# Kernel tuning notes

Hardware: AMD Instinct MI355X
Metric: run time of the kernel (lower is better)

The kernel has to match this reference:

```python
import jax, jax.numpy as jnp
import numpy as np

B, T, H, S, OBS, ACT = 64, 256, 1024, 128, 1024, 32


def setup_inputs() -> dict:
    key = jax.random.key(0)
    ks = jax.random.split(key, 9)
    w = lambda k, shape, fan_in: jax.random.normal(k, shape, jnp.float32) / np.sqrt(fan_in).astype(np.float32)
    return {
        "obs": jax.random.normal(ks[0], (B, T, OBS), jnp.float32),
        "action": jax.random.normal(ks[1], (B, T, ACT), jnp.float32),
        "resets": jnp.zeros((B,), jnp.bool_),
        "noise": jax.random.normal(ks[2], (B, T, S), jnp.float32),
        # GRUCell params (PyTorch layout: gates ordered r,z,n)
        "w_ih": w(ks[3], (3 * H, S + ACT), S + ACT),
        "w_hh": w(ks[4], (3 * H, H), H),
        "b_ih": jnp.zeros((3 * H,), jnp.float32),
        "b_hh": jnp.zeros((3 * H,), jnp.float32),
        # prior MLP: H -> H//2 -> 2S
        "pr_w1": w(ks[5], (H // 2, H), H),
        "pr_b1": jnp.zeros((H // 2,), jnp.float32),
        "pr_w2": w(ks[6], (2 * S, H // 2), H // 2),
        "pr_b2": jnp.zeros((2 * S,), jnp.float32),
        # posterior MLP: (H+OBS) -> (H+OBS)//2 -> 2S
        "po_w1": w(ks[7], ((H + OBS) // 2, H + OBS), H + OBS),
        "po_b1": jnp.zeros(((H + OBS) // 2,), jnp.float32),
        "po_w2": w(ks[8], (2 * S, (H + OBS) // 2), (H + OBS) // 2),
        "po_b2": jnp.zeros((2 * S,), jnp.float32),
    }


def reference(obs, action, resets, noise, w_ih, w_hh, b_ih, b_hh,
              pr_w1, pr_b1, pr_w2, pr_b2, po_w1, po_b1, po_w2, po_b2):
    Bv, Tv, _ = obs.shape
    keep = (~resets).astype(obs.dtype)[:, None]  # [B,1]; multiplies h,z for t>0
    # prev_action: zeros at t=0, action[:, t-1] afterwards
    prev_act = jnp.concatenate([jnp.zeros_like(action[:, :1]), action[:, :-1]], axis=1)

    def step(carry, xs):
        h, z = carry
        a_t, o_t, n_t, t_pos = xs
        m = jnp.where(t_pos > 0, keep, jnp.ones_like(keep))
        h = h * m
        z = z * m
        x = jnp.concatenate([z, a_t], axis=-1)
        gi = x @ w_ih.T + b_ih
        gh = h @ w_hh.T + b_hh
        ir, iz, inn = jnp.split(gi, 3, axis=-1)
        hr, hz, hn = jnp.split(gh, 3, axis=-1)
        r = jax.nn.sigmoid(ir + hr)
        u = jax.nn.sigmoid(iz + hz)
        n = jnp.tanh(inn + r * hn)
        h = (1.0 - u) * n + u * h
        pp = jax.nn.relu(h @ pr_w1.T + pr_b1) @ pr_w2.T + pr_b2
        pm, ps = jnp.split(pp, 2, axis=-1)
        ps = jax.nn.softplus(ps) + 1e-6
        qp = jax.nn.relu(jnp.concatenate([h, o_t], axis=-1) @ po_w1.T + po_b1) @ po_w2.T + po_b2
        qm, qs = jnp.split(qp, 2, axis=-1)
        qs = jax.nn.softplus(qs) + 1e-6
        z = qm + qs * n_t  # reparameterized rsample
        return (h, z), (h, z, pm, ps, qm, qs)

    h0 = jnp.zeros((Bv, w_hh.shape[-1]), obs.dtype)
    z0 = jnp.zeros((Bv, noise.shape[-1]), obs.dtype)
    xs = (jnp.swapaxes(prev_act, 0, 1), jnp.swapaxes(obs, 0, 1),
          jnp.swapaxes(noise, 0, 1), jnp.arange(Tv))
    _, (hs, zs, pm, ps, qm, qs) = jax.lax.scan(step, (h0, z0), xs)
    h_seq = jnp.swapaxes(hs, 0, 1)  # [B,T,H]
    z_seq = jnp.swapaxes(zs, 0, 1)  # [B,T,S]
    to_last = lambda a: jnp.moveaxis(a, 0, -1)  # torch stacks dists along dim=-1 -> [B,S,T]
    return (to_last(pm), to_last(ps), to_last(qm), to_last(qs), h_seq, z_seq)
```

## Files before the change

### kernel.cpp

```cpp
#include <hip/hip_runtime.h>

#define B_ 64
#define T_ 256
#define H_ 1024
#define S_ 128
#define OBS_ 1024
#define ACT_ 32

typedef __attribute__((ext_vector_type(8))) short bf16x8;
typedef __attribute__((ext_vector_type(4))) float f32x4;

#define MFMA(a, b, c) __builtin_amdgcn_mfma_f32_16x16x32_bf16((a), (b), (c), 0, 0, 0)

__device__ __forceinline__ float bf2f(short s) {
    unsigned int u = ((unsigned int)(unsigned short)s) << 16;
    float f; __builtin_memcpy(&f, &u, 4); return f;
}
__device__ __forceinline__ short f2bf(float f) {
    unsigned int u; __builtin_memcpy(&u, &f, 4);
    unsigned int r = (u + 0x7fffu + ((u >> 16) & 1u)) >> 16;
    return (short)r;
}
__device__ __forceinline__ bf16x8 ld8(const short* p) { return *(const bf16x8*)p; }
__device__ __forceinline__ bf16x8 cvt8(const float* p) {
    bf16x8 r;
#pragma unroll
    for (int i = 0; i < 8; ++i) r[i] = f2bf(p[i]);
    return r;
}
__device__ __forceinline__ void sta8(short* p, unsigned long long v) {
    __hip_atomic_store((unsigned long long*)p, v, __ATOMIC_RELAXED, __HIP_MEMORY_SCOPE_AGENT);
}
__device__ __forceinline__ unsigned long long pk4(float4 v) {
    return (unsigned long long)(unsigned short)f2bf(v.x)
         | ((unsigned long long)(unsigned short)f2bf(v.y) << 16)
         | ((unsigned long long)(unsigned short)f2bf(v.z) << 32)
         | ((unsigned long long)(unsigned short)f2bf(v.w) << 48);
}
__device__ __forceinline__ float sigm(float x) { return 1.f / (1.f + __expf(-x)); }
__device__ __forceinline__ float tanh_f(float x) { return 1.f - 2.f / (__expf(2.f * x) + 1.f); }
__device__ __forceinline__ float splus(float x) { return (x > 20.f) ? x : log1pf(__expf(x)); }

__device__ __forceinline__ void gridbar(int* flags, int e) {
    __syncthreads();
    if (threadIdx.x == 0)
        __hip_atomic_store(&flags[blockIdx.x * 16], e, __ATOMIC_RELAXED, __HIP_MEMORY_SCOPE_AGENT);
    if (threadIdx.x < 64) {
        while (__hip_atomic_load(&flags[threadIdx.x * 16], __ATOMIC_RELAXED,
                                 __HIP_MEMORY_SCOPE_AGENT) < e)
            __builtin_amdgcn_s_sleep(1);
    }
    __builtin_amdgcn_fence(__ATOMIC_ACQUIRE, "agent");
    __syncthreads();
}

__global__ void f2bf_arr(const float* __restrict__ src, short* __restrict__ dst, int n4) {
    int i = blockIdx.x * blockDim.x + threadIdx.x;
    if (i < n4) {
        float4 v = ((const float4*)src)[i];
        short4 o;
        o.x = f2bf(v.x); o.y = f2bf(v.y); o.z = f2bf(v.z); o.w = f2bf(v.w);
        ((short4*)dst)[i] = o;
    }
}

__global__ __launch_bounds__(256) void obs_gemm(
    const float* __restrict__ obs, const short* __restrict__ po_w1,
    const float* __restrict__ po_b1, short* __restrict__ part) {
    const int t = blockIdx.x;
    const int rg = threadIdx.x >> 6, lane = threadIdx.x & 63;
    const int c = lane & 15, q = lane >> 4;
    bf16x8 afr[32];
    const float* ap = obs + ((size_t)(rg * 16 + c) * T_ + t) * OBS_;
#pragma unroll
    for (int kb = 0; kb < 32; ++kb) afr[kb] = cvt8(ap + kb * 32 + q * 8);
    for (int jt = 0; jt < 64; ++jt) {
        f32x4 acc = {0.f, 0.f, 0.f, 0.f};
        const short* wgt = po_w1 + (size_t)(jt * 16 + c) * 2048 + 1024;
#pragma unroll 8
        for (int kb = 0; kb < 32; ++kb) acc = MFMA(afr[kb], ld8(wgt + kb * 32 + q * 8), acc);
        const float bias = po_b1[jt * 16 + c];
#pragma unroll
        for (int e = 0; e < 4; ++e) {
            const int br = rg * 16 + q * 4 + e;
            part[((size_t)t * 64 + br) * 1024 + jt * 16 + c] = f2bf(acc[e] + bias);
        }
    }
}

__global__ __launch_bounds__(256, 1) void rssm_scan(
    const short* __restrict__ act_bf, const unsigned char* __restrict__ resets,
    const short* __restrict__ w_ih, const short* __restrict__ w_hh,
    const float* __restrict__ b_ih, const float* __restrict__ b_hh,
    const short* __restrict__ po_w1, const short* __restrict__ po_w2,
    const float* __restrict__ po_b2, const short* __restrict__ part,
    const float* __restrict__ noise,
    int* flags, short* h_bf, short* z_bf, short* poh,
    float* __restrict__ out_h, float* __restrict__ out_qm,
    float* __restrict__ out_qs, float* __restrict__ out_z) {
    extern __shared__ __align__(16) char smem[];
    bf16x8* wlds = (bf16x8*)smem;
    __shared__ __align__(16) float stg[64][20];
    const int tid = threadIdx.x, bid = blockIdx.x;
    const int rg = tid >> 6, lane = tid & 63, c = lane & 15, q = lane >> 4;
    const int j0 = bid * 16, m0 = rg * 16, arow = m0 + c, n = j0 + c;
    const int srow = tid >> 2, sseg = tid & 3;
    const bf16x8 zv8 = {0, 0, 0, 0, 0, 0, 0, 0};

    for (int i = 0; i < 32; ++i) {
        const int fid = i * 256 + tid;
        const int g = fid >> 11, kb = (fid >> 6) & 31, ln = fid & 63;
        const int cc = ln & 15, qq = ln >> 4;
        const short* src = (g == 0)
            ? po_w1 + (size_t)(j0 + cc) * 2048 + kb * 32 + qq * 8
            : w_hh + (size_t)((g - 1) * 1024 + j0 + cc) * 1024 + kb * 32 + qq * 8;
        wlds[fid] = ld8(src);
    }
    bf16x8* wih = wlds + 8192;
    for (int f = tid; f < 960; f += 256) {
        const int g = f / 320, rem = f % 320, kk = rem >> 6, ln = rem & 63;
        const int cc = ln & 15, qq = ln >> 4;
        wih[f] = ld8(w_ih + (size_t)(g * 1024 + j0 + cc) * 160 + kk * 32 + qq * 8);
    }
    __syncthreads();

    const bool rsA = resets[arow] != 0;
    bool rsR[4];
#pragma unroll
    for (int e = 0; e < 4; ++e) rsR[e] = resets[m0 + q * 4 + e] != 0;
    const float biR = b_ih[n], bhR = b_hh[n];
    const float biU = b_ih[1024 + n], bhU = b_hh[1024 + n];
    const float biN = b_ih[2048 + n], bhN = b_hh[2048 + n];
    const short* ha = h_bf + arow * 1024;
    const bf16x8* wPl = wlds;
    const bf16x8* wRl = wlds + 2048;
    const bf16x8* wUl = wlds + 4096;
    const bf16x8* wNl = wlds + 6144;
    const bf16x8* wiRl = wih;
    const bf16x8* wiUl = wih + 320;
    const bf16x8* wiNl = wih + 640;
    const int s2 = (bid < 8) ? j0 + c : 0;
    const short* wm = po_w2 + (size_t)s2 * 1024;
    const short* ws2 = po_w2 + (size_t)(128 + s2) * 1024;
    const float bM = (bid < 8) ? po_b2[s2] : 0.f;
    const float bS = (bid < 8) ? po_b2[128 + s2] : 0.f;

    f32x4 hp = {0.f, 0.f, 0.f, 0.f};
    f32x4 gR = {0.f, 0.f, 0.f, 0.f};
    f32x4 gU = {0.f, 0.f, 0.f, 0.f};
    f32x4 gN = {0.f, 0.f, 0.f, 0.f};
    f32x4 pinit;
#pragma unroll
    for (int e = 0; e < 4; ++e)
        pinit[e] = bf2f(part[((size_t)0 * 64 + m0 + q * 4 + e) * 1024 + n]);

    int ep = 1;
    for (int t = 0; t < T_; ++t) {
        f32x4 iR = {0.f, 0.f, 0.f, 0.f};
        f32x4 iU = iR, iN = iR;
        if (t > 0) {
            const short* za = z_bf + arow * 128;
            bf16x8 zfr[4];
#pragma unroll
            for (int kb = 0; kb < 4; ++kb) zfr[kb] = ld8(za + kb * 32 + q * 8);
            bf16x8 a2 = ld8(act_bf + (size_t)arow * (T_ * ACT_) + (size_t)(t - 1) * ACT_ + q * 8);
#pragma unroll
            for (int kb = 0; kb < 4; ++kb) {
                bf16x8 a = rsA ? zv8 : zfr[kb];
                iR = MFMA(a, wiRl[kb * 64 + lane], iR);
                iU = MFMA(a, wiUl[kb * 64 + lane], iU);
                iN = MFMA(a, wiNl[kb * 64 + lane], iN);
            }
            iR = MFMA(a2, wiRl[256 + lane], iR);
            iU = MFMA(a2, wiUl[256 + lane], iU);
            iN = MFMA(a2, wiNl[256 + lane], iN);
        }
#pragma unroll
        for (int e = 0; e < 4; ++e) {
            const float hpv = (t > 0 && rsR[e]) ? 0.f : hp[e];
            const float r = sigm(iR[e] + gR[e] + biR + bhR);
            const float u = sigm(iU[e] + gU[e] + biU + bhU);
            const float nn = tanh_f(iN[e] + biN + r * (gN[e] + bhN));
            const float hv = (1.f - u) * nn + u * hpv;
            hp[e] = hv;
            stg[m0 + q * 4 + e][c] = hv;
        }
        __syncthreads();
        {
            float4 hv4 = *(const float4*)&stg[srow][sseg * 4];
            sta8(h_bf + srow * 1024 + j0 + sseg * 4, pk4(hv4));
            *(float4*)(out_h + (size_t)srow * (T_ * H_) + (size_t)t * H_ + j0 + sseg * 4) = hv4;
        }
        gridbar(flags, ep++);
        float nz[4];
        {
            bf16x8 hfr[32];
#pragma unroll
            for (int kb = 0; kb < 32; ++kb) hfr[kb] = ld8(ha + kb * 32 + q * 8);
            f32x4 accP = pinit;
            if (t + 1 < T_) {
#pragma unroll
                for (int e = 0; e < 4; ++e)
                    pinit[e] = bf2f(part[((size_t)(t + 1) * 64 + m0 + q * 4 + e) * 1024 + n]);
            }
            if (bid < 8) {
#pragma unroll
                for (int e = 0; e < 4; ++e)
                    nz[e] = noise[(size_t)(m0 + q * 4 + e) * (T_ * S_) + (size_t)t * S_ + s2];
            }
            f32x4 nR = {0.f, 0.f, 0.f, 0.f};
            f32x4 nU = nR, nN = nR;
#pragma unroll 8
            for (int kb = 0; kb < 32; ++kb) {
                bf16x8 a = hfr[kb];
                bf16x8 am = rsA ? zv8 : a;
                accP = MFMA(a, wPl[kb * 64 + lane], accP);
                nR = MFMA(am, wRl[kb * 64 + lane], nR);
                nU = MFMA(am, wUl[kb * 64 + lane], nU);
                nN = MFMA(am, wNl[kb * 64 + lane], nN);
            }
            gR = nR; gU = nU; gN = nN;
#pragma unroll
            for (int e = 0; e < 4; ++e) stg[m0 + q * 4 + e][c] = fmaxf(accP[e], 0.f);
        }
        __syncthreads();
        {
            float4 v4 = *(const float4*)&stg[srow][sseg * 4];
            sta8(poh + srow * 1024 + j0 + sseg * 4, pk4(v4));
        }
        gridbar(flags, ep++);
        if (bid < 8) {
            bf16x8 pfr[32];
            const short* pa = poh + arow * 1024;
#pragma unroll
            for (int kb = 0; kb < 32; ++kb) pfr[kb] = ld8(pa + kb * 32 + q * 8);
            f32x4 aM = {0.f, 0.f, 0.f, 0.f};
            f32x4 aS = aM;
#pragma unroll 8
            for (int kb = 0; kb < 32; ++kb) {
                aM = MFMA(pfr[kb], ld8(wm + kb * 32 + q * 8), aM);
                aS = MFMA(pfr[kb], ld8(ws2 + kb * 32 + q * 8), aS);
            }
#pragma unroll
            for (int e = 0; e < 4; ++e) {
                const int row = m0 + q * 4 + e;
                const float qm = aM[e] + bM;
                const float qs = splus(aS[e] + bS) + 1e-6f;
                stg[row][c] = qm + qs * nz[e];
                out_qm[(size_t)row * (S_ * T_) + (size_t)s2 * T_ + t] = qm;
                out_qs[(size_t)row * (S_ * T_) + (size_t)s2 * T_ + t] = qs;
            }
            __syncthreads();
            {
                float4 z4 = *(const float4*)&stg[srow][sseg * 4];
                *(float4*)(out_z + (size_t)srow * (T_ * S_) + (size_t)t * S_ + j0 + sseg * 4) = z4;
                sta8(z_bf + srow * 128 + j0 + sseg * 4, pk4(z4));
            }
        }
        gridbar(flags, ep++);
    }
}

__global__ __launch_bounds__(256) void prior_mlp(
    const float* __restrict__ hseq, const short* __restrict__ pr_w1,
    const float* __restrict__ pr_b1, const short* __restrict__ pr_w2,
    const float* __restrict__ pr_b2, float* __restrict__ out_pm,
    float* __restrict__ out_ps) {
    __shared__ __align__(16) short hid[64][512];
    const int w = threadIdx.x >> 6;
    const int lane = threadIdx.x & 63;
    const int c = lane & 15, q = lane >> 4;
    const long rb0 = (long)blockIdx.x * 64;
    bf16x8 afr[32];
    const float* ap = hseq + (rb0 + w * 16 + c) * 1024;
#pragma unroll
    for (int kb = 0; kb < 32; ++kb) afr[kb] = cvt8(ap + kb * 32 + q * 8);
    for (int jt = 0; jt < 32; ++jt) {
        f32x4 acc = {0.f, 0.f, 0.f, 0.f};
        const short* wgt = pr_w1 + (size_t)(jt * 16 + c) * 1024;
#pragma unroll 8
        for (int kb = 0; kb < 32; ++kb) acc = MFMA(afr[kb], ld8(wgt + kb * 32 + q * 8), acc);
        const float bias = pr_b1[jt * 16 + c];
#pragma unroll
        for (int e = 0; e < 4; ++e)
            hid[w * 16 + q * 4 + e][jt * 16 + c] = f2bf(fmaxf(acc[e] + bias, 0.f));
    }
    __syncthreads();
    bf16x8 afr2[16];
#pragma unroll
    for (int kb = 0; kb < 16; ++kb) afr2[kb] = *(const bf16x8*)(&hid[w * 16 + c][kb * 32 + q * 8]);
    for (int jt = 0; jt < 16; ++jt) {
        f32x4 acc = {0.f, 0.f, 0.f, 0.f};
        const short* wgt = pr_w2 + (size_t)(jt * 16 + c) * 512;
#pragma unroll 8
        for (int kb = 0; kb < 16; ++kb) acc = MFMA(afr2[kb], ld8(wgt + kb * 32 + q * 8), acc);
        const int col = jt * 16 + c;
#pragma unroll
        for (int e = 0; e < 4; ++e) {
            const long rgidx = rb0 + w * 16 + q * 4 + e;
            const int b_ = (int)(rgidx >> 8), t_ = (int)(rgidx & 255);
            if (col < S_) {
                out_pm[(size_t)b_ * (S_ * T_) + (size_t)col * T_ + t_] = acc[e] + pr_b2[col];
            } else {
                out_ps[(size_t)b_ * (S_ * T_) + (size_t)(col - S_) * T_ + t_] =
                    splus(acc[e] + pr_b2[col]) + 1e-6f;
            }
        }
    }
}

extern "C" void kernel_launch(void* const* d_in, const int* in_sizes, int n_in,
                              void* d_out, int out_size, void* d_ws, size_t ws_size,
                              hipStream_t stream) {
    const float* obs = (const float*)d_in[0];
    const float* action = (const float*)d_in[1];
    const unsigned char* resets = (const unsigned char*)d_in[2];
    const float* noise = (const float*)d_in[3];
    const float* w_ih = (const float*)d_in[4];
    const float* w_hh = (const float*)d_in[5];
    const float* b_ih = (const float*)d_in[6];
    const float* b_hh = (const float*)d_in[7];
    const float* pr_w1 = (const float*)d_in[8];
    const float* pr_b1 = (const float*)d_in[9];
    const float* pr_w2 = (const float*)d_in[10];
    const float* pr_b2 = (const float*)d_in[11];
    const float* po_w1 = (const float*)d_in[12];
    const float* po_b1 = (const float*)d_in[13];
    const float* po_w2 = (const float*)d_in[14];
    const float* po_b2 = (const float*)d_in[15];

    float* out = (float*)d_out;
    const size_t BST = (size_t)B_ * S_ * T_;
    float* out_pm = out;
    float* out_ps = out + BST;
    float* out_qm = out + 2 * BST;
    float* out_qs = out + 3 * BST;
    float* out_h = out + 4 * BST;
    float* out_z = out + 4 * BST + (size_t)B_ * T_ * H_;

    char* w = (char*)d_ws;
    int* flags = (int*)w;
    short* h_bf = (short*)(w + 4096);
    short* z_bf = (short*)(w + 266240);
    short* poh = (short*)(w + 282624);
    short* act_bf = (short*)(w + 413696);
    short* w_ih_bf = (short*)(w + 1462272);
    short* w_hh_bf = (short*)(w + 2445312);
    short* po_w1_bf = (short*)(w + 8736768);
    short* po_w2_bf = (short*)(w + 12931072);
    short* pr_w1_bf = (short*)(w + 13455360);
    short* pr_w2_bf = (short*)(w + 14503936);
    short* part = (short*)(w + 14766080);

    static bool attr_set = false;
    if (!attr_set) {
        hipFuncSetAttribute(reinterpret_cast<const void*>(&rssm_scan),
                            hipFuncAttributeMaxDynamicSharedMemorySize, 146432);
        attr_set = true;
    }

    auto cvt = [&](const float* s, short* d, int n) {
        int n4 = n / 4;
        f2bf_arr<<<dim3((n4 + 255) / 256), 256, 0, stream>>>(s, d, n4);
    };
    cvt(action, act_bf, B_ * T_ * ACT_);
    cvt(w_ih, w_ih_bf, 3 * H_ * (S_ + ACT_));
    cvt(w_hh, w_hh_bf, 3 * H_ * H_);
    cvt(po_w1, po_w1_bf, 1024 * 2048);
    cvt(po_w2, po_w2_bf, 256 * 1024);
    cvt(pr_w1, pr_w1_bf, 512 * 1024);
    cvt(pr_w2, pr_w2_bf, 256 * 512);

    obs_gemm<<<dim3(256), 256, 0, stream>>>(obs, po_w1_bf, po_b1, part);

    rssm_scan<<<dim3(64), 256, 146432, stream>>>(
        act_bf, resets, w_ih_bf, w_hh_bf, b_ih, b_hh,
        po_w1_bf, po_w2_bf, po_b2, part, noise,
        flags, h_bf, z_bf, poh, out_h, out_qm, out_qs, out_z);

    prior_mlp<<<dim3(256), 256, 0, stream>>>(out_h, pr_w1_bf, pr_b1, pr_w2_bf, pr_b2,
                                             out_pm, out_ps);
}
```

Before: 11.93 ms.

## Drop grid-barrier acquire fence and stage posterior outputs for a separate transpose

Removes the agent-scope acquire fence from the software grid barrier. In its place, the cross-block buffers (h, z, posterior hidden) are read with relaxed agent-scope atomic loads, which avoids a cache invalidation at every one of the many per-step barriers. The strided per-timestep qm/qs stores inside the serial scan become contiguous writes into a staging buffer. That buffer reuses the already-consumed slice of the precomputed obs-projection buffer. A new transpose kernel then writes them to the [B,S,T] layout, which adds a launch and extra traffic but moves the scattered stores off the critical path. Correctness now depends on every cross-block read going through the atomic path and on the buffer aliasing order.

```diff
diff --git a/kernel.cpp b/kernel.cpp
--- a/kernel.cpp
+++ b/kernel.cpp
@@ -27,6 +27,13 @@
 #pragma unroll
     for (int i = 0; i < 8; ++i) r[i] = f2bf(p[i]);
     return r;
+}
+__device__ __forceinline__ bf16x8 lda8(const short* p) {
+    const unsigned long long* q8 = (const unsigned long long*)p;
+    union { unsigned long long q[2]; bf16x8 v; } u;
+    u.q[0] = __hip_atomic_load(q8, __ATOMIC_RELAXED, __HIP_MEMORY_SCOPE_AGENT);
+    u.q[1] = __hip_atomic_load(q8 + 1, __ATOMIC_RELAXED, __HIP_MEMORY_SCOPE_AGENT);
+    return u.v;
 }
 __device__ __forceinline__ void sta8(short* p, unsigned long long v) {
     __hip_atomic_store((unsigned long long*)p, v, __ATOMIC_RELAXED, __HIP_MEMORY_SCOPE_AGENT);
@@ -50,7 +57,6 @@
                                  __HIP_MEMORY_SCOPE_AGENT) < e)
             __builtin_amdgcn_s_sleep(1);
     }
-    __builtin_amdgcn_fence(__ATOMIC_ACQUIRE, "agent");
     __syncthreads();
 }
 
@@ -93,11 +99,10 @@
     const short* __restrict__ w_ih, const short* __restrict__ w_hh,
     const float* __restrict__ b_ih, const float* __restrict__ b_hh,
     const short* __restrict__ po_w1, const short* __restrict__ po_w2,
-    const float* __restrict__ po_b2, const short* __restrict__ part,
+    const float* __restrict__ po_b2, const short* part, float* qbuf,
     const float* __restrict__ noise,
     int* flags, short* h_bf, short* z_bf, short* poh,
-    float* __restrict__ out_h, float* __restrict__ out_qm,
-    float* __restrict__ out_qs, float* __restrict__ out_z) {
+    float* __restrict__ out_h, float* __restrict__ out_z) {
     extern __shared__ __align__(16) char smem[];
     bf16x8* wlds = (bf16x8*)smem;
     __shared__ __align__(16) float stg[64][20];
@@ -162,7 +167,7 @@
             const short* za = z_bf + arow * 128;
             bf16x8 zfr[4];
 #pragma unroll
-            for (int kb = 0; kb < 4; ++kb) zfr[kb] = ld8(za + kb * 32 + q * 8);
+            for (int kb = 0; kb < 4; ++kb) zfr[kb] = lda8(za + kb * 32 + q * 8);
             bf16x8 a2 = ld8(act_bf + (size_t)arow * (T_ * ACT_) + (size_t)(t - 1) * ACT_ + q * 8);
 #pragma unroll
             for (int kb = 0; kb < 4; ++kb) {
@@ -196,7 +201,7 @@
         {
             bf16x8 hfr[32];
 #pragma unroll
-            for (int kb = 0; kb < 32; ++kb) hfr[kb] = ld8(ha + kb * 32 + q * 8);
+            for (int kb = 0; kb < 32; ++kb) hfr[kb] = lda8(ha + kb * 32 + q * 8);
             f32x4 accP = pinit;
             if (t + 1 < T_) {
 #pragma unroll
@@ -233,7 +238,7 @@
             bf16x8 pfr[32];
             const short* pa = poh + arow * 1024;
 #pragma unroll
-            for (int kb = 0; kb < 32; ++kb) pfr[kb] = ld8(pa + kb * 32 + q * 8);
+            for (int kb = 0; kb < 32; ++kb) pfr[kb] = lda8(pa + kb * 32 + q * 8);
             f32x4 aM = {0.f, 0.f, 0.f, 0.f};
             f32x4 aS = aM;
 #pragma unroll 8
@@ -241,14 +246,15 @@
                 aM = MFMA(pfr[kb], ld8(wm + kb * 32 + q * 8), aM);
                 aS = MFMA(pfr[kb], ld8(ws2 + kb * 32 + q * 8), aS);
             }
+            float* qb = qbuf + (size_t)t * 32768;
 #pragma unroll
             for (int e = 0; e < 4; ++e) {
                 const int row = m0 + q * 4 + e;
                 const float qm = aM[e] + bM;
                 const float qs = splus(aS[e] + bS) + 1e-6f;
                 stg[row][c] = qm + qs * nz[e];
-                out_qm[(size_t)row * (S_ * T_) + (size_t)s2 * T_ + t] = qm;
-                out_qs[(size_t)row * (S_ * T_) + (size_t)s2 * T_ + t] = qs;
+                qb[row * 256 + s2] = qm;
+                qb[row * 256 + 128 + s2] = qs;
             }
             __syncthreads();
             {
@@ -258,6 +264,32 @@
             }
         }
         gridbar(flags, ep++);
+    }
+}
+
+__global__ __launch_bounds__(256) void qtrans(
+    const char* qbase, float* __restrict__ out_qm, float* __restrict__ out_qs) {
+    __shared__ float tile[64][129];
+    const int b = blockIdx.x & 63, tb = blockIdx.x >> 6;
+    const int t0 = tb * 64;
+    const int sA = threadIdx.x & 127, th = threadIdx.x >> 7;
+    const int tw = threadIdx.x & 63, sw = threadIdx.x >> 6;
+    for (int pass = 0; pass < 2; ++pass) {
+        const int coff = pass * 128;
+#pragma unroll 4
+        for (int i = 0; i < 32; ++i) {
+            const int tt = i * 2 + th;
+            const float* src = (const float*)(qbase + (size_t)(t0 + tt) * 131072);
+            tile[tt][sA] = src[b * 256 + coff + sA];
+        }
+        __syncthreads();
+        float* dst = pass ? out_qs : out_qm;
+#pragma unroll 4
+        for (int j = 0; j < 32; ++j) {
+            const int s = j * 4 + sw;
+            dst[(size_t)b * (S_ * T_) + (size_t)s * T_ + t0 + tw] = tile[tw][s];
+        }
+        __syncthreads();
     }
 }
 
@@ -351,6 +383,7 @@
     short* pr_w1_bf = (short*)(w + 13455360);
     short* pr_w2_bf = (short*)(w + 14503936);
     short* part = (short*)(w + 14766080);
+    float* qbuf = (float*)part;
 
     static bool attr_set = false;
     if (!attr_set) {
@@ -375,8 +408,10 @@
 
     rssm_scan<<<dim3(64), 256, 146432, stream>>>(
         act_bf, resets, w_ih_bf, w_hh_bf, b_ih, b_hh,
-        po_w1_bf, po_w2_bf, po_b2, part, noise,
-        flags, h_bf, z_bf, poh, out_h, out_qm, out_qs, out_z);
+        po_w1_bf, po_w2_bf, po_b2, part, qbuf, noise,
+        flags, h_bf, z_bf, poh, out_h, out_z);
+
+    qtrans<<<dim3(256), 256, 0, stream>>>((const char*)qbuf, out_qm, out_qs);
 
     prior_mlp<<<dim3(256), 256, 0, stream>>>(out_h, pr_w1_bf, pr_b1, pr_w2_bf, pr_b2,
                                              out_pm, out_ps);
```

After: 12.23 ms. 1.03x slower.

## Drop grid-barrier acquire fence, use volatile loads for shared state, stream w_ih from global

Applied to the files above, without the earlier changes.

The agent-scope acquire fence in the grid barrier is removed. Loads of the cross-block h, z and posterior-hidden buffers become volatile 64-bit loads so they still bypass stale cache without a full fence. The w_ih slice is no longer staged in LDS and is read straight from global memory each step, which lowers the dynamic shared memory request. The aim is to shorten each per-step barrier; the cost is more global traffic for w_ih and a weaker memory-ordering guarantee that may not be correct on this hardware.

```diff
diff --git a/kernel.cpp b/kernel.cpp
--- a/kernel.cpp
+++ b/kernel.cpp
@@ -27,6 +27,13 @@
 #pragma unroll
     for (int i = 0; i < 8; ++i) r[i] = f2bf(p[i]);
     return r;
+}
+__device__ __forceinline__ bf16x8 ldv8(const short* p) {
+    const volatile unsigned long long* q8 = (const volatile unsigned long long*)p;
+    union { unsigned long long q[2]; bf16x8 v; } u;
+    u.q[0] = q8[0];
+    u.q[1] = q8[1];
+    return u.v;
 }
 __device__ __forceinline__ void sta8(short* p, unsigned long long v) {
     __hip_atomic_store((unsigned long long*)p, v, __ATOMIC_RELAXED, __HIP_MEMORY_SCOPE_AGENT);
@@ -50,7 +57,6 @@
                                  __HIP_MEMORY_SCOPE_AGENT) < e)
             __builtin_amdgcn_s_sleep(1);
     }
-    __builtin_amdgcn_fence(__ATOMIC_ACQUIRE, "agent");
     __syncthreads();
 }
 
@@ -116,18 +122,15 @@
             : w_hh + (size_t)((g - 1) * 1024 + j0 + cc) * 1024 + kb * 32 + qq * 8;
         wlds[fid] = ld8(src);
     }
-    bf16x8* wih = wlds + 8192;
-    for (int f = tid; f < 960; f += 256) {
-        const int g = f / 320, rem = f % 320, kk = rem >> 6, ln = rem & 63;
-        const int cc = ln & 15, qq = ln >> 4;
-        wih[f] = ld8(w_ih + (size_t)(g * 1024 + j0 + cc) * 160 + kk * 32 + qq * 8);
-    }
     __syncthreads();
 
     const bool rsA = resets[arow] != 0;
     bool rsR[4];
 #pragma unroll
     for (int e = 0; e < 4; ++e) rsR[e] = resets[m0 + q * 4 + e] != 0;
+    const short* wiR = w_ih + (size_t)n * 160;
+    const short* wiU = w_ih + (size_t)(1024 + n) * 160;
+    const short* wiN = w_ih + (size_t)(2048 + n) * 160;
     const float biR = b_ih[n], bhR = b_hh[n];
     const float biU = b_ih[1024 + n], bhU = b_hh[1024 + n];
     const float biN = b_ih[2048 + n], bhN = b_hh[2048 + n];
@@ -136,9 +139,6 @@
     const bf16x8* wRl = wlds + 2048;
     const bf16x8* wUl = wlds + 4096;
     const bf16x8* wNl = wlds + 6144;
-    const bf16x8* wiRl = wih;
-    const bf16x8* wiUl = wih + 320;
-    const bf16x8* wiNl = wih + 640;
     const int s2 = (bid < 8) ? j0 + c : 0;
     const short* wm = po_w2 + (size_t)s2 * 1024;
     const short* ws2 = po_w2 + (size_t)(128 + s2) * 1024;
@@ -162,18 +162,19 @@
             const short* za = z_bf + arow * 128;
             bf16x8 zfr[4];
 #pragma unroll
-            for (int kb = 0; kb < 4; ++kb) zfr[kb] = ld8(za + kb * 32 + q * 8);
+            for (int kb = 0; kb < 4; ++kb) zfr[kb] = ldv8(za + kb * 32 + q * 8);
             bf16x8 a2 = ld8(act_bf + (size_t)arow * (T_ * ACT_) + (size_t)(t - 1) * ACT_ + q * 8);
 #pragma unroll
             for (int kb = 0; kb < 4; ++kb) {
+                const int kk = kb * 32 + q * 8;
                 bf16x8 a = rsA ? zv8 : zfr[kb];
-                iR = MFMA(a, wiRl[kb * 64 + lane], iR);
-                iU = MFMA(a, wiUl[kb * 64 + lane], iU);
-                iN = MFMA(a, wiNl[kb * 64 + lane], iN);
-            }
-            iR = MFMA(a2, wiRl[256 + lane], iR);
-            iU = MFMA(a2, wiUl[256 + lane], iU);
-            iN = MFMA(a2, wiNl[256 + lane], iN);
+                iR = MFMA(a, ld8(wiR + kk), iR);
+                iU = MFMA(a, ld8(wiU + kk), iU);
+                iN = MFMA(a, ld8(wiN + kk), iN);
+            }
+            iR = MFMA(a2, ld8(wiR + 128 + q * 8), iR);
+            iU = MFMA(a2, ld8(wiU + 128 + q * 8), iU);
+            iN = MFMA(a2, ld8(wiN + 128 + q * 8), iN);
         }
 #pragma unroll
         for (int e = 0; e < 4; ++e) {
@@ -196,7 +197,7 @@
         {
             bf16x8 hfr[32];
 #pragma unroll
-            for (int kb = 0; kb < 32; ++kb) hfr[kb] = ld8(ha + kb * 32 + q * 8);
+            for (int kb = 0; kb < 32; ++kb) hfr[kb] = ldv8(ha + kb * 32 + q * 8);
             f32x4 accP = pinit;
             if (t + 1 < T_) {
 #pragma unroll
@@ -233,7 +234,7 @@
             bf16x8 pfr[32];
             const short* pa = poh + arow * 1024;
 #pragma unroll
-            for (int kb = 0; kb < 32; ++kb) pfr[kb] = ld8(pa + kb * 32 + q * 8);
+            for (int kb = 0; kb < 32; ++kb) pfr[kb] = ldv8(pa + kb * 32 + q * 8);
             f32x4 aM = {0.f, 0.f, 0.f, 0.f};
             f32x4 aS = aM;
 #pragma unroll 8
@@ -355,7 +356,7 @@
     static bool attr_set = false;
     if (!attr_set) {
         hipFuncSetAttribute(reinterpret_cast<const void*>(&rssm_scan),
-                            hipFuncAttributeMaxDynamicSharedMemorySize, 146432);
+                            hipFuncAttributeMaxDynamicSharedMemorySize, 131072);
         attr_set = true;
     }
 
@@ -373,7 +374,7 @@
 
     obs_gemm<<<dim3(256), 256, 0, stream>>>(obs, po_w1_bf, po_b1, part);
 
-    rssm_scan<<<dim3(64), 256, 146432, stream>>>(
+    rssm_scan<<<dim3(64), 256, 131072, stream>>>(
         act_bf, resets, w_ih_bf, w_hh_bf, b_ih, b_hh,
         po_w1_bf, po_w2_bf, po_b2, part, noise,
         flags, h_bf, z_bf, poh, out_h, out_qm, out_qs, out_z);
```

After: 14.16 ms. 1.19x slower.
